# Kernel optimization log

Measured on AMD Instinct MI355X. Metric: run time of the kernel, lower is better.

Reference implementation:

```python
import jax, jax.numpy as jnp
import numpy as np

D_MODEL = 1024
N_HEADS = 16


def setup_inputs() -> dict:
    key = jax.random.key(0)
    ks = jax.random.split(key, 5)
    B, T, C = 4, 2048, D_MODEL
    x = jax.random.normal(ks[0], (B, T, C), dtype=jnp.float32)
    s = 1.0 / np.sqrt(C)
    W_attn = jax.random.normal(ks[1], (C, 3 * C), dtype=jnp.float32) * s
    b_attn = jnp.zeros((3 * C,), dtype=jnp.float32)
    W_proj = jax.random.normal(ks[2], (C, C), dtype=jnp.float32) * s
    b_proj = jnp.zeros((C,), dtype=jnp.float32)
    return {"x": x, "W_attn": W_attn, "b_attn": b_attn, "W_proj": W_proj, "b_proj": b_proj}


def reference(x, W_attn, b_attn, W_proj, b_proj):
    B, T, C = x.shape
    H = N_HEADS
    hd = C // H
    qkv = x @ W_attn + b_attn                      # [B,T,3C]
    q, k, v = jnp.split(qkv, 3, axis=-1)
    # reshape to [B,H,T,hd]
    q = q.reshape(B, T, H, hd).transpose(0, 2, 1, 3)
    k = k.reshape(B, T, H, hd).transpose(0, 2, 1, 3)
    v = v.reshape(B, T, H, hd).transpose(0, 2, 1, 3)
    scale = 1.0 / jnp.sqrt(jnp.asarray(hd, dtype=x.dtype))
    aff = jnp.einsum('bhqd,bhkd->bhqk', q, k) * scale   # [B,H,T,T]
    causal = jnp.tril(jnp.ones((T, T), dtype=bool))
    aff = jnp.where(causal, aff, jnp.asarray(-jnp.inf, dtype=aff.dtype))
    p = jax.nn.softmax(aff, axis=-1)
    y = jnp.einsum('bhqk,bhkd->bhqd', p, v)             # [B,H,T,hd]
    y = y.transpose(0, 2, 1, 3).reshape(B, T, C)
    return y @ W_proj + b_proj
```

## Files before the change

kernel.cpp:

```cpp
#include <hip/hip_runtime.h>
#include <stdint.h>
#include <math.h>

typedef __attribute__((ext_vector_type(8))) __bf16 bf16x8;
typedef __attribute__((ext_vector_type(4))) __bf16 bf16x4;
typedef __attribute__((ext_vector_type(4))) float f32x4;
typedef __attribute__((ext_vector_type(16))) float f32x16;

#define MFMA16(A, B, C) __builtin_amdgcn_mfma_f32_16x16x32_bf16((A), (B), (C), 0, 0, 0)
#define MFMA32(A, B, C) __builtin_amdgcn_mfma_f32_32x32x16_bf16((A), (B), (C), 0, 0, 0)

#if defined(__has_builtin)
#if __has_builtin(__builtin_amdgcn_exp2f)
#define EXP2(x) __builtin_amdgcn_exp2f(x)
#else
#define EXP2(x) exp2f(x)
#endif
#else
#define EXP2(x) exp2f(x)
#endif

static constexpr int kT  = 2048;
static constexpr int kC  = 1024;
static constexpr int kHD = 64;
#define QSCALE 0.1803368801111204f

__device__ __forceinline__ void g2l16(const void* g, void* l) {
  __builtin_amdgcn_global_load_lds(
      (const __attribute__((address_space(1))) uint32_t*)g,
      (__attribute__((address_space(3))) uint32_t*)l, 16, 0, 0);
}

__global__ __launch_bounds__(256) void k_convert_x(const float* __restrict__ x,
                                                   __bf16* __restrict__ xb) {
  int i = (blockIdx.x * 256 + threadIdx.x) * 4;
  f32x4 v = *(const f32x4*)(x + i);
  bf16x4 o;
  o[0] = (__bf16)v[0]; o[1] = (__bf16)v[1]; o[2] = (__bf16)v[2]; o[3] = (__bf16)v[3];
  *(bf16x4*)(xb + i) = o;
}

__global__ __launch_bounds__(256) void k_transpose_w(const float* __restrict__ src,
                                                     __bf16* __restrict__ dst, int N) {
  __shared__ float t[32][33];
  int k0 = blockIdx.x * 32, n0 = blockIdx.y * 32;
  int c = threadIdx.x & 31, r = threadIdx.x >> 5;
#pragma unroll
  for (int i = 0; i < 4; ++i)
    t[r + i * 8][c] = src[(size_t)(k0 + r + i * 8) * N + n0 + c];
  __syncthreads();
#pragma unroll
  for (int i = 0; i < 4; ++i)
    dst[(size_t)(n0 + r + i * 8) * 1024 + k0 + c] = (__bf16)t[c][r + i * 8];
}

static constexpr int GK = 1024;
static constexpr int GNT = GK / 32;

template <int MODE>
__global__ __launch_bounds__(256, 3) void k_gemm(const __bf16* __restrict__ A,
                                                 const __bf16* __restrict__ Bw,
                                                 const float* __restrict__ bias,
                                                 __bf16* __restrict__ qo,
                                                 __bf16* __restrict__ ko,
                                                 __bf16* __restrict__ vo,
                                                 float* __restrict__ out) {
  __shared__ __bf16 As[3][128 * 32];
  __shared__ __bf16 Bs[3][128 * 32];

  const int tid = threadIdx.x;
  const int wave = tid >> 6, lane = tid & 63;
  const int lo = lane & 15, hi = lane >> 4;
  const int wr = wave & 1, wc = wave >> 1;

  constexpr int NBN = (MODE == 0) ? 24 : 8;
  const int nwg = (int)gridDim.x;
  const int id = (int)blockIdx.x;
  const int wg = (id & 7) * (nwg >> 3) + (id >> 3);
  const int bm = wg / NBN, bn = wg % NBN;
  const int m0 = bm * 128, n0 = bn * 128;

  const int rG0 = tid >> 2, gG0 = (tid & 3) ^ ((rG0 >> 1) & 3);
  const int rG1 = (tid + 256) >> 2, gG1 = ((tid + 256) & 3) ^ ((rG1 >> 1) & 3);
  const __bf16* gaA0 = A + (size_t)(m0 + rG0) * GK + gG0 * 8;
  const __bf16* gaA1 = A + (size_t)(m0 + rG1) * GK + gG1 * 8;
  const __bf16* gbB0 = Bw + (size_t)(n0 + rG0) * GK + gG0 * 8;
  const __bf16* gbB1 = Bw + (size_t)(n0 + rG1) * GK + gG1 * 8;

  const int fsw = (hi ^ ((lo >> 1) & 3)) * 8;
  const int offA = (wr * 64 + lo) * 32 + fsw;
  const int offB = (wc * 64 + lo) * 32 + fsw;

  f32x4 acc[4][4] = {};

#define GSTAGE(jt, bufi)                                  \
  {                                                       \
    g2l16(gaA0 + (jt) * 32, &As[(bufi)][tid * 8]);        \
    g2l16(gaA1 + (jt) * 32, &As[(bufi)][2048 + tid * 8]); \
    g2l16(gbB0 + (jt) * 32, &Bs[(bufi)][tid * 8]);        \
    g2l16(gbB1 + (jt) * 32, &Bs[(bufi)][2048 + tid * 8]); \
  }

#define GMFMA(RB)                                                            \
  {                                                                          \
    bf16x8 af[4], bfr[4];                                                    \
    _Pragma("unroll")                                                        \
    for (int m = 0; m < 4; ++m)                                              \
      af[m] = *(const bf16x8*)&As[RB][offA + m * 512];                       \
    _Pragma("unroll")                                                        \
    for (int n = 0; n < 4; ++n)                                              \
      bfr[n] = *(const bf16x8*)&Bs[RB][offB + n * 512];                      \
    __builtin_amdgcn_s_setprio(1);                                           \
    _Pragma("unroll")                                                        \
    for (int m = 0; m < 4; ++m)                                              \
      _Pragma("unroll")                                                      \
      for (int n = 0; n < 4; ++n)                                            \
        acc[m][n] = MFMA16(af[m], bfr[n], acc[m][n]);                        \
    __builtin_amdgcn_s_setprio(0);                                           \
  }

#define GITER(RB, RS, JT)                          \
  {                                                \
    GSTAGE((JT) + 2, RS);                          \
    GMFMA(RB);                                     \
    asm volatile("s_waitcnt vmcnt(4)" ::: "memory"); \
    __builtin_amdgcn_s_barrier();                  \
    __builtin_amdgcn_sched_barrier(0);             \
  }

  GSTAGE(0, 0);
  GSTAGE(1, 1);
  asm volatile("s_waitcnt vmcnt(4)" ::: "memory");
  __builtin_amdgcn_s_barrier();
  __builtin_amdgcn_sched_barrier(0);

#pragma unroll 1
  for (int j = 0; j < GNT - 2; j += 3) {
    GITER(0, 2, j);
    GITER(1, 0, j + 1);
    GITER(2, 1, j + 2);
  }
  GMFMA(0);
  asm volatile("s_waitcnt vmcnt(0)" ::: "memory");
  __builtin_amdgcn_s_barrier();
  __builtin_amdgcn_sched_barrier(0);
  GMFMA(1);

#undef GITER
#undef GMFMA
#undef GSTAGE

  if (MODE == 0) {
#pragma unroll
    for (int nj = 0; nj < 4; ++nj) {
      int gn = n0 + wc * 64 + nj * 16 + lo;
      float bv = bias[gn];
      int which = gn >> 10;
      int c = gn & 1023;
      int hh = c >> 6, d = c & 63;
#pragma unroll
      for (int mi = 0; mi < 4; ++mi) {
        int gm = m0 + wr * 64 + mi * 16 + hi * 4;
        int bb = gm >> 11, t0 = gm & 2047;
        if (which == 2) {
          int t0p = t0 ^ ((((t0 >> 2) ^ (t0 >> 3)) & 1) * 12);
          bf16x4 vv;
#pragma unroll
          for (int r = 0; r < 4; ++r) vv[r] = (__bf16)(acc[mi][nj][r] + bv);
          *(bf16x4*)(vo + ((size_t)(bb * 16 + hh) * 64 + d) * 2048 + t0p) = vv;
        } else {
#pragma unroll
          for (int r = 0; r < 4; ++r) {
            float val = acc[mi][nj][r] + bv;
            size_t idx = (((size_t)(bb * 16 + hh)) * 2048 + (t0 + r)) * 64 + d;
            if (which == 0)
              qo[idx] = (__bf16)(val * QSCALE);
            else
              ko[idx] = (__bf16)val;
          }
        }
      }
    }
  } else {
#pragma unroll
    for (int nj = 0; nj < 4; ++nj) {
      int gn = n0 + wc * 64 + nj * 16 + lo;
      float bv = bias[gn];
#pragma unroll
      for (int mi = 0; mi < 4; ++mi) {
        int gm = m0 + wr * 64 + mi * 16 + hi * 4;
#pragma unroll
        for (int r = 0; r < 4; ++r)
          out[(size_t)(gm + r) * 1024 + gn] = acc[mi][nj][r] + bv;
      }
    }
  }
}

__global__ __launch_bounds__(256, 2) void k_flash(const __bf16* __restrict__ qb,
                                                  const __bf16* __restrict__ kb,
                                                  const __bf16* __restrict__ vt,
                                                  __bf16* __restrict__ ob) {
  __shared__ __bf16 Ks[2][64 * 64];
  __shared__ __bf16 Vs[2][64 * 64];

  const int id = (int)blockIdx.x;
  const int xcd = id & 7, jj = id >> 3;
  const int bh = (jj & 7) * 8 + xcd;
  const int xsi = jj >> 3;
  const int xs = (xsi < 4) ? xsi : 11 - xsi;
  const int b = bh >> 4, h = bh & 15;
  const int tid = threadIdx.x, wave = tid >> 6, lane = tid & 63;
  const int l31 = lane & 31, hi32 = lane >> 5;
  const int gx = l31 & 7;

  const int qrow[2] = { (15 - xs) * 128 + wave * 32, xs * 128 + wave * 32 };

  bf16x8 qf[2][4];
#pragma unroll
  for (int rg = 0; rg < 2; ++rg) {
    const __bf16* Qp = qb + ((size_t)bh * kT + qrow[rg] + l31) * kHD + hi32 * 8;
#pragma unroll
    for (int ks = 0; ks < 4; ++ks)
      qf[rg][ks] = *(const bf16x8*)(Qp + ks * 16);
  }

  f32x16 acc[2][2] = {};
  float srow[2] = {0.0f, 0.0f};

  const __bf16* Kbase = kb + (size_t)bh * kT * kHD;
  const __bf16* Vbase = vt + (size_t)bh * kHD * kT;

  int srcK[2], srcV[2];
#pragma unroll
  for (int p = 0; p < 2; ++p) {
    int g = wave * 64 + lane + p * 256;
    int r = g >> 3, c = g & 7;
    int cs = c ^ (r & 7);
    srcK[p] = r * kHD + cs * 8;
    srcV[p] = r * kT + cs * 8;
  }

  const int nt = 32 - 2 * xs;

#pragma unroll
  for (int p = 0; p < 2; ++p) {
    g2l16(Kbase + srcK[p], &Ks[0][wave * 512 + p * 2048]);
    g2l16(Vbase + srcV[p], &Vs[0][wave * 512 + p * 2048]);
  }

  for (int it = 0; it < nt; ++it) {
    const int kt = it * 64;
    const int pb = it & 1;
    const bool both = (it <= 2 * xs + 1);

    __syncthreads();

    if (it + 1 < nt) {
      const int kn = kt + 64;
#pragma unroll
      for (int p = 0; p < 2; ++p) {
        g2l16(Kbase + kn * kHD + srcK[p], &Ks[1 - pb][wave * 512 + p * 2048]);
        g2l16(Vbase + kn + srcV[p],       &Vs[1 - pb][wave * 512 + p * 2048]);
      }
    }

    const __bf16* Kt = &Ks[pb][0];
    const __bf16* Vt = &Vs[pb][0];

    bf16x8 pa[2][4];

#pragma unroll
    for (int kb2 = 0; kb2 < 2; ++kb2) {
      bf16x8 ka[4];
#pragma unroll
      for (int ks = 0; ks < 4; ++ks)
        ka[ks] = *(const bf16x8*)&Kt[(kb2 * 32 + l31) * 64 +
                                     (((ks * 2 + hi32) ^ gx) * 8)];
#pragma unroll
      for (int rg = 0; rg < 2; ++rg) {
        if (rg == 1 && !both) break;
        f32x16 s = {};
        __builtin_amdgcn_s_setprio(1);
#pragma unroll
        for (int ks = 0; ks < 4; ++ks) s = MFMA32(ka[ks], qf[rg][ks], s);
        __builtin_amdgcn_s_setprio(0);
        const int qg = qrow[rg] + l31;
        const int kbs = kt + kb2 * 32 + 4 * hi32;
        if (kt + kb2 * 32 + 31 > qrow[rg]) {
#pragma unroll
          for (int i = 0; i < 16; ++i)
            if (kbs + (i & 3) + 8 * (i >> 2) > qg) s[i] = -INFINITY;
        }
#pragma unroll
        for (int i = 0; i < 16; ++i) s[i] = EXP2(s[i]);
        float sm = 0.0f;
#pragma unroll
        for (int i = 0; i < 16; ++i) sm += s[i];
        srow[rg] += sm;
#pragma unroll
        for (int a = 0; a < 2; ++a) {
          bf16x8 p;
#pragma unroll
          for (int e = 0; e < 8; ++e) p[e] = (__bf16)s[8 * a + e];
          pa[rg][kb2 * 2 + a] = p;
        }
      }
    }

    __builtin_amdgcn_s_setprio(1);
#pragma unroll
    for (int db = 0; db < 2; ++db) {
#pragma unroll
      for (int ks = 0; ks < 4; ++ks) {
        bf16x8 vb = *(const bf16x8*)&Vt[(db * 32 + l31) * 64 +
                                        (((ks * 2 + hi32) ^ gx) * 8)];
        acc[0][db] = MFMA32(pa[0][ks], vb, acc[0][db]);
        if (both) acc[1][db] = MFMA32(pa[1][ks], vb, acc[1][db]);
      }
    }
    __builtin_amdgcn_s_setprio(0);
  }

#pragma unroll
  for (int rg = 0; rg < 2; ++rg) {
    float tot = srow[rg] + __shfl_xor(srow[rg], 32, 64);
    float invt = 1.0f / tot;
    __bf16* Op = ob + ((size_t)b * kT + qrow[rg]) * kC + h * kHD;
#pragma unroll
    for (int i = 0; i < 16; ++i) {
      int q = (i & 3) + 8 * (i >> 2) + 4 * hi32;
      float inv = __shfl(invt, q, 64);
      Op[(size_t)q * kC + l31]      = (__bf16)(acc[rg][0][i] * inv);
      Op[(size_t)q * kC + 32 + l31] = (__bf16)(acc[rg][1][i] * inv);
    }
  }
}

extern "C" void kernel_launch(void* const* d_in, const int* in_sizes, int n_in,
                              void* d_out, int out_size, void* d_ws, size_t ws_size,
                              hipStream_t stream) {
  const float* x      = (const float*)d_in[0];
  const float* W_attn = (const float*)d_in[1];
  const float* b_attn = (const float*)d_in[2];
  const float* W_proj = (const float*)d_in[3];
  const float* b_proj = (const float*)d_in[4];
  float* out = (float*)d_out;

  char* ws = (char*)d_ws;
  __bf16* xb  = (__bf16*)(ws + 0);
  __bf16* ob  = (__bf16*)(ws + 0);
  __bf16* wab = (__bf16*)(ws + 16777216);
  __bf16* wpb = (__bf16*)(ws + 23068672);
  __bf16* qbf = (__bf16*)(ws + 25165824);
  __bf16* kbf = (__bf16*)(ws + 41943040);
  __bf16* vtb = (__bf16*)(ws + 58720256);

  k_convert_x<<<8192, 256, 0, stream>>>(x, xb);
  k_transpose_w<<<dim3(32, 96), 256, 0, stream>>>(W_attn, wab, 3072);
  k_transpose_w<<<dim3(32, 32), 256, 0, stream>>>(W_proj, wpb, 1024);
  k_gemm<0><<<dim3(1536), 256, 0, stream>>>(xb, wab, b_attn, qbf, kbf, vtb, nullptr);
  k_flash<<<dim3(512), 256, 0, stream>>>(qbf, kbf, vtb, ob);
  k_gemm<1><<<dim3(512), 256, 0, stream>>>(ob, wpb, b_proj, nullptr, nullptr, nullptr, out);
}
```

Before: 238.2 us.

## Triple-buffer flash K/V loads and merge prep kernels into one launch

The flash attention kernel moves from a double-buffered K/V tile pipeline to a three-stage ring, prefetching two tiles ahead. A single barrier after the compute, guarded by explicit vmcnt waits, replaces the per-iteration __syncthreads, so global-to-LDS loads can overlap more compute. The x conversion and both weight transposes are also fused into one launch to cut launch overhead. LDS use per block grows from 32KB to 48KB, which may limit occupancy at two blocks per CU, and the wait counts have to match the number of outstanding loads exactly.

```diff
diff --git a/kernel.cpp b/kernel.cpp
--- a/kernel.cpp
+++ b/kernel.cpp
@@ -31,20 +31,29 @@
       (__attribute__((address_space(3))) uint32_t*)l, 16, 0, 0);
 }
 
-__global__ __launch_bounds__(256) void k_convert_x(const float* __restrict__ x,
-                                                   __bf16* __restrict__ xb) {
-  int i = (blockIdx.x * 256 + threadIdx.x) * 4;
-  f32x4 v = *(const f32x4*)(x + i);
-  bf16x4 o;
-  o[0] = (__bf16)v[0]; o[1] = (__bf16)v[1]; o[2] = (__bf16)v[2]; o[3] = (__bf16)v[3];
-  *(bf16x4*)(xb + i) = o;
-}
-
-__global__ __launch_bounds__(256) void k_transpose_w(const float* __restrict__ src,
-                                                     __bf16* __restrict__ dst, int N) {
+__global__ __launch_bounds__(256) void k_prep(const float* __restrict__ x,
+                                              __bf16* __restrict__ xb,
+                                              const float* __restrict__ Wa,
+                                              __bf16* __restrict__ wab,
+                                              const float* __restrict__ Wp,
+                                              __bf16* __restrict__ wpb) {
+  const int bid = (int)blockIdx.x;
+  const int tid = threadIdx.x;
+  if (bid < 8192) {
+    int i = (bid * 256 + tid) * 4;
+    f32x4 v = *(const f32x4*)(x + i);
+    bf16x4 o;
+    o[0] = (__bf16)v[0]; o[1] = (__bf16)v[1]; o[2] = (__bf16)v[2]; o[3] = (__bf16)v[3];
+    *(bf16x4*)(xb + i) = o;
+    return;
+  }
   __shared__ float t[32][33];
-  int k0 = blockIdx.x * 32, n0 = blockIdx.y * 32;
-  int c = threadIdx.x & 31, r = threadIdx.x >> 5;
+  int tb = bid - 8192;
+  const float* src; __bf16* dst; int N;
+  if (tb < 3072) { src = Wa; dst = wab; N = 3072; }
+  else           { tb -= 3072; src = Wp; dst = wpb; N = 1024; }
+  const int k0 = (tb & 31) * 32, n0 = (tb >> 5) * 32;
+  const int c = tid & 31, r = tid >> 5;
 #pragma unroll
   for (int i = 0; i < 4; ++i)
     t[r + i * 8][c] = src[(size_t)(k0 + r + i * 8) * N + n0 + c];
@@ -119,13 +128,13 @@
     __builtin_amdgcn_s_setprio(0);                                           \
   }
 
-#define GITER(RB, RS, JT)                          \
-  {                                                \
-    GSTAGE((JT) + 2, RS);                          \
-    GMFMA(RB);                                     \
+#define GITER(RB, RS, JT)                            \
+  {                                                  \
+    GSTAGE((JT) + 2, RS);                            \
+    GMFMA(RB);                                       \
     asm volatile("s_waitcnt vmcnt(4)" ::: "memory"); \
-    __builtin_amdgcn_s_barrier();                  \
-    __builtin_amdgcn_sched_barrier(0);             \
+    __builtin_amdgcn_s_barrier();                    \
+    __builtin_amdgcn_sched_barrier(0);               \
   }
 
   GSTAGE(0, 0);
@@ -201,8 +210,8 @@
                                                   const __bf16* __restrict__ kb,
                                                   const __bf16* __restrict__ vt,
                                                   __bf16* __restrict__ ob) {
-  __shared__ __bf16 Ks[2][64 * 64];
-  __shared__ __bf16 Vs[2][64 * 64];
+  __shared__ __bf16 Ks[3][64 * 64];
+  __shared__ __bf16 Vs[3][64 * 64];
 
   const int id = (int)blockIdx.x;
   const int xcd = id & 7, jj = id >> 3;
@@ -248,25 +257,31 @@
     g2l16(Kbase + srcK[p], &Ks[0][wave * 512 + p * 2048]);
     g2l16(Vbase + srcV[p], &Vs[0][wave * 512 + p * 2048]);
   }
-
+#pragma unroll
+  for (int p = 0; p < 2; ++p) {
+    g2l16(Kbase + 64 * kHD + srcK[p], &Ks[1][wave * 512 + p * 2048]);
+    g2l16(Vbase + 64 + srcV[p],       &Vs[1][wave * 512 + p * 2048]);
+  }
+  asm volatile("s_waitcnt vmcnt(4)" ::: "memory");
+  __builtin_amdgcn_s_barrier();
+  __builtin_amdgcn_sched_barrier(0);
+
+  int rb = 0, rs = 2;
   for (int it = 0; it < nt; ++it) {
     const int kt = it * 64;
-    const int pb = it & 1;
     const bool both = (it <= 2 * xs + 1);
 
-    __syncthreads();
-
-    if (it + 1 < nt) {
-      const int kn = kt + 64;
+    if (it + 2 < nt) {
+      const int kn = kt + 128;
 #pragma unroll
       for (int p = 0; p < 2; ++p) {
-        g2l16(Kbase + kn * kHD + srcK[p], &Ks[1 - pb][wave * 512 + p * 2048]);
-        g2l16(Vbase + kn + srcV[p],       &Vs[1 - pb][wave * 512 + p * 2048]);
-      }
-    }
-
-    const __bf16* Kt = &Ks[pb][0];
-    const __bf16* Vt = &Vs[pb][0];
+        g2l16(Kbase + kn * kHD + srcK[p], &Ks[rs][wave * 512 + p * 2048]);
+        g2l16(Vbase + kn + srcV[p],       &Vs[rs][wave * 512 + p * 2048]);
+      }
+    }
+
+    const __bf16* Kt = &Ks[rb][0];
+    const __bf16* Vt = &Vs[rb][0];
 
     bf16x8 pa[2][4];
 
@@ -320,6 +335,18 @@
       }
     }
     __builtin_amdgcn_s_setprio(0);
+
+    if (it + 2 < nt) {
+      asm volatile("s_waitcnt vmcnt(4)" ::: "memory");
+    } else if (it + 2 == nt) {
+      asm volatile("s_waitcnt vmcnt(0)" ::: "memory");
+    }
+    if (it + 1 < nt) {
+      __builtin_amdgcn_s_barrier();
+      __builtin_amdgcn_sched_barrier(0);
+    }
+    rb = (rb == 2) ? 0 : rb + 1;
+    rs = (rs == 2) ? 0 : rs + 1;
   }
 
 #pragma unroll
@@ -356,9 +383,7 @@
   __bf16* kbf = (__bf16*)(ws + 41943040);
   __bf16* vtb = (__bf16*)(ws + 58720256);
 
-  k_convert_x<<<8192, 256, 0, stream>>>(x, xb);
-  k_transpose_w<<<dim3(32, 96), 256, 0, stream>>>(W_attn, wab, 3072);
-  k_transpose_w<<<dim3(32, 32), 256, 0, stream>>>(W_proj, wpb, 1024);
+  k_prep<<<12288, 256, 0, stream>>>(x, xb, W_attn, wab, W_proj, wpb);
   k_gemm<0><<<dim3(1536), 256, 0, stream>>>(xb, wab, b_attn, qbf, kbf, vtb, nullptr);
   k_flash<<<dim3(512), 256, 0, stream>>>(qbf, kbf, vtb, ob);
   k_gemm<1><<<dim3(512), 256, 0, stream>>>(ob, wpb, b_proj, nullptr, nullptr, nullptr, out);
```

Result: no change. 237.7 us (-0.2%).
